# Performance work log

Measured on AMD Instinct MI355X. Metric: run time of the kernel, lower is better.

## Reference

```python
import jax, jax.numpy as jnp
import numpy as np

WS = 7          # window size (odd)
NUM_HEADS = 4


def _indices(H, W, ws):
    """Replicates get_attn_idx / get_bias_idx from the torch module (static numpy)."""
    H_, W_ = H - (ws - 1), W - (ws - 1)
    pad = ws // 2
    # unfold idx: flat key indices of each ws x ws window anchored at valid positions
    h_idx = np.tile(np.arange(W_), H_)
    w_idx = np.repeat(np.arange(H_), W_) * W
    k_idx = np.tile(np.arange(ws), ws) + np.repeat(np.arange(ws), ws) * W
    unfold = (h_idx + w_idx)[:, None] + k_idx            # [H_*W_, ws^2]
    # replication-pad the map of valid-window ids to size H x W
    amap = np.arange(H_ * W_).reshape(H_, W_)
    amap = np.pad(amap, pad, mode='edge').reshape(-1)    # [H*W]
    attn_idx = unfold[amap]                              # [H*W, ws^2]
    # relative-position bias indices
    nh = np.ones(ws, dtype=np.int64); nh[pad] = H - (ws - 1)
    nw = np.ones(ws, dtype=np.int64); nw[pad] = W - (ws - 1)
    ih = np.repeat(np.arange(ws), nh)                    # [H]
    iw = np.repeat(np.arange(ws), nw)                    # [W]
    idx_k = (np.arange(ws)[:, None] * (2 * ws - 1) + np.arange(ws)).reshape(-1)
    bias_hw = ih[:, None] * (2 * ws - 1) + iw            # [H, W]
    bias_idx = (bias_hw[..., None] + idx_k).reshape(-1, ws * ws)  # [H*W, ws^2]
    return jnp.asarray(attn_idx, jnp.int32), jnp.asarray(bias_idx, jnp.int32)


def setup_inputs() -> dict:
    key = jax.random.key(0)
    ks = jax.random.split(key, 6)
    B, C, H, W = 2, 64, 128, 128
    return {
        'x': jax.random.normal(ks[0], (B, C, H, W), jnp.float32),
        'qkv_w': jax.random.normal(ks[1], (3 * C, C), jnp.float32) * 0.05,
        'qkv_b': jax.random.normal(ks[2], (3 * C,), jnp.float32) * 0.05,
        'proj_w': jax.random.normal(ks[3], (C, C), jnp.float32) * 0.05,
        'proj_b': jax.random.normal(ks[4], (C,), jnp.float32) * 0.05,
        'relative_bias': jax.random.normal(ks[5], ((2 * WS - 1) ** 2, NUM_HEADS), jnp.float32) * 0.02,
    }


def reference(x, qkv_w, qkv_b, proj_w, proj_b, relative_bias):
    B, C, H, W = x.shape
    nH = NUM_HEADS
    hd = C // nH
    scale = hd ** -0.5
    attn_idx, bias_idx = _indices(H, W, WS)   # static int constants

    # 1x1 conv qkv
    qkv = jnp.einsum('bchw,oc->bohw', x, qkv_w) + qkv_b[None, :, None, None]
    qkv = qkv.reshape(B, 3, nH, hd, H * W)
    q = qkv[:, 0].transpose(0, 1, 3, 2) * scale          # [B,nH,HW,hd]
    k = qkv[:, 1].transpose(0, 1, 3, 2)
    v = qkv[:, 2].transpose(0, 1, 3, 2)

    kg = k[:, :, attn_idx]                               # [B,nH,HW,ws^2,hd]
    bias = relative_bias[bias_idx].transpose(2, 0, 1)    # [nH,HW,ws^2]
    attn = jnp.einsum('bhnd,bhnkd->bhnk', q, kg) + bias[None]
    attn = jax.nn.softmax(attn, axis=-1)

    out = jnp.einsum('bhnk,bhnkd->bhnd', attn, v[:, :, attn_idx])  # [B,nH,HW,hd]
    out = out.transpose(0, 1, 3, 2).reshape(B, C, H, W)

    out = jnp.einsum('bchw,oc->bohw', out, proj_w) + proj_b[None, :, None, None]
    return out
```

## Files before the change

kernel.cpp:

```cpp
#include <hip/hip_runtime.h>

#define HW 16384
#define NH 4
#define HD 16

__global__ __launch_bounds__(256) void qkv_kernel(
    const float* __restrict__ x, const float* __restrict__ w,
    const float* __restrict__ bias, float* __restrict__ qT,
    float* __restrict__ kT, float* __restrict__ vT)
{
  __shared__ float xs[64][72];
  int slice = blockIdx.x;
  int p0    = blockIdx.y * 64;
  int b     = blockIdx.z;
  int t     = threadIdx.x;

  {
    int c = t >> 2, f4 = t & 3;
    const float4* src = (const float4*)(x + (size_t)(b * 64 + c) * HW + p0);
    float4* dst = (float4*)(&xs[c][0]);
#pragma unroll
    for (int k2 = 0; k2 < 4; ++k2) dst[f4 * 4 + k2] = src[f4 * 4 + k2];
  }
  __syncthreads();

  int px = t & 63;
  int wv  = __builtin_amdgcn_readfirstlane(t >> 6);
  int o16 = slice * 4 + wv;
  int o0  = o16 * 16;
  int tsel = o16 >> 2;
  int h    = o16 & 3;

  float acc[16];
#pragma unroll
  for (int d = 0; d < 16; ++d) acc[d] = bias[o0 + d];

  for (int c4 = 0; c4 < 16; ++c4) {
    float a0 = xs[c4 * 4 + 0][px];
    float a1 = xs[c4 * 4 + 1][px];
    float a2 = xs[c4 * 4 + 2][px];
    float a3 = xs[c4 * 4 + 3][px];
#pragma unroll
    for (int d = 0; d < 16; ++d) {
      const float* wr = w + (o0 + d) * 64 + c4 * 4;
      acc[d] = fmaf(wr[0], a0, acc[d]);
      acc[d] = fmaf(wr[1], a1, acc[d]);
      acc[d] = fmaf(wr[2], a2, acc[d]);
      acc[d] = fmaf(wr[3], a3, acc[d]);
    }
  }
  if (tsel == 0) {
#pragma unroll
    for (int d = 0; d < 16; ++d) acc[d] *= 0.25f;
  }
  float* dst = (tsel == 0) ? qT : ((tsel == 1) ? kT : vT);
  float4* dp = (float4*)(dst + ((size_t)(b * NH + h) * HW + p0 + px) * HD);
  dp[0] = make_float4(acc[0], acc[1], acc[2], acc[3]);
  dp[1] = make_float4(acc[4], acc[5], acc[6], acc[7]);
  dp[2] = make_float4(acc[8], acc[9], acc[10], acc[11]);
  dp[3] = make_float4(acc[12], acc[13], acc[14], acc[15]);
}


__device__ __forceinline__ float4* swzp(float* buf, int px, int d4) {
  int off = (px << 6) ^ (((px & 7) ^ d4) << 4);
  return (float4*)((char*)buf + off);
}
__device__ __forceinline__ const float4* swzpc(const float* buf, int px, int d4) {
  int off = (px << 6) ^ (((px & 7) ^ d4) << 4);
  return (const float4*)((const char*)buf + off);
}

__global__ __launch_bounds__(256) void attn_kernel(
    const float* __restrict__ qT, const float* __restrict__ kT,
    const float* __restrict__ vT, const float* __restrict__ rb,
    float* __restrict__ attO)
{
  __shared__ float KV[484 * 16];
  __shared__ float rbl[169];

  int tile = blockIdx.x;
  int h    = blockIdx.y;
  int b    = blockIdx.z;
  int tx0  = (tile & 7) * 16;
  int ty0  = (tile >> 3) * 16;
  int oy   = ty0 - 3, ox = tx0 - 3;
  int t    = threadIdx.x;

  size_t base = (size_t)(b * NH + h) * HW;

  if (t < 169) rbl[t] = rb[t * NH + h];

  for (int idx = t; idx < 1936; idx += 256) {
    int pxi = idx >> 2, d4 = idx & 3;
    int r = pxi / 22, c = pxi % 22;
    int ra = oy + r; ra = ra < 0 ? 0 : (ra > 127 ? 127 : ra);
    int ca = ox + c; ca = ca < 0 ? 0 : (ca > 127 ? 127 : ca);
    size_t gp = (base + (size_t)ra * 128 + ca) * HD;
    *swzp(KV, pxi, d4) = ((const float4*)(kT + gp))[d4];
  }

  int lx = t & 15, ly = t >> 4;
  int y = ty0 + ly, xc = tx0 + lx;
  int sy = y - 3;  sy = sy < 0 ? 0 : (sy > 121 ? 121 : sy);
  int sx = xc - 3; sx = sx < 0 ? 0 : (sx > 121 ? 121 : sx);
  int li0 = sy - oy, lj0 = sx - ox;
  int ih = y - sy, iw = xc - sx;

  float qd[16];
  {
    const float4* qp = (const float4*)(qT + (base + (size_t)y * 128 + xc) * HD);
#pragma unroll
    for (int k = 0; k < 4; ++k) {
      float4 v = qp[k];
      qd[4 * k + 0] = v.x; qd[4 * k + 1] = v.y;
      qd[4 * k + 2] = v.z; qd[4 * k + 3] = v.w;
    }
  }

  __syncthreads();

  float lg[49];
#pragma unroll
  for (int i = 0; i < 7; ++i) {
#pragma unroll
    for (int j = 0; j < 7; ++j) {
      int px = (li0 + i) * 22 + (lj0 + j);
      float4 k0 = *swzpc(KV, px, 0);
      float4 k1 = *swzpc(KV, px, 1);
      float4 k2 = *swzpc(KV, px, 2);
      float4 k3 = *swzpc(KV, px, 3);
      float d;
      d = fmaf(qd[0], k0.x, rbl[(ih + i) * 13 + (iw + j)]);
      d = fmaf(qd[1], k0.y, d);  d = fmaf(qd[2], k0.z, d);
      d = fmaf(qd[3], k0.w, d);  d = fmaf(qd[4], k1.x, d);
      d = fmaf(qd[5], k1.y, d);  d = fmaf(qd[6], k1.z, d);
      d = fmaf(qd[7], k1.w, d);  d = fmaf(qd[8], k2.x, d);
      d = fmaf(qd[9], k2.y, d);  d = fmaf(qd[10], k2.z, d);
      d = fmaf(qd[11], k2.w, d); d = fmaf(qd[12], k3.x, d);
      d = fmaf(qd[13], k3.y, d); d = fmaf(qd[14], k3.z, d);
      d = fmaf(qd[15], k3.w, d);
      lg[i * 7 + j] = d;
    }
  }

  float mx = lg[0];
#pragma unroll
  for (int k = 1; k < 49; ++k) mx = fmaxf(mx, lg[k]);
  float s = 0.f;
#pragma unroll
  for (int k = 0; k < 49; ++k) { lg[k] = __expf(lg[k] - mx); s += lg[k]; }
  float inv = 1.f / s;

  __syncthreads();
  for (int idx = t; idx < 1936; idx += 256) {
    int pxi = idx >> 2, d4 = idx & 3;
    int r = pxi / 22, c = pxi % 22;
    int ra = oy + r; ra = ra < 0 ? 0 : (ra > 127 ? 127 : ra);
    int ca = ox + c; ca = ca < 0 ? 0 : (ca > 127 ? 127 : ca);
    size_t gp = (base + (size_t)ra * 128 + ca) * HD;
    *swzp(KV, pxi, d4) = ((const float4*)(vT + gp))[d4];
  }
  __syncthreads();

  float4 o0 = make_float4(0,0,0,0), o1 = o0, o2 = o0, o3 = o0;
#pragma unroll
  for (int i = 0; i < 7; ++i) {
#pragma unroll
    for (int j = 0; j < 7; ++j) {
      int px = (li0 + i) * 22 + (lj0 + j);
      float p = lg[i * 7 + j];
      float4 v0 = *swzpc(KV, px, 0);
      float4 v1 = *swzpc(KV, px, 1);
      float4 v2 = *swzpc(KV, px, 2);
      float4 v3 = *swzpc(KV, px, 3);
      o0.x = fmaf(p, v0.x, o0.x); o0.y = fmaf(p, v0.y, o0.y);
      o0.z = fmaf(p, v0.z, o0.z); o0.w = fmaf(p, v0.w, o0.w);
      o1.x = fmaf(p, v1.x, o1.x); o1.y = fmaf(p, v1.y, o1.y);
      o1.z = fmaf(p, v1.z, o1.z); o1.w = fmaf(p, v1.w, o1.w);
      o2.x = fmaf(p, v2.x, o2.x); o2.y = fmaf(p, v2.y, o2.y);
      o2.z = fmaf(p, v2.z, o2.z); o2.w = fmaf(p, v2.w, o2.w);
      o3.x = fmaf(p, v3.x, o3.x); o3.y = fmaf(p, v3.y, o3.y);
      o3.z = fmaf(p, v3.z, o3.z); o3.w = fmaf(p, v3.w, o3.w);
    }
  }

  size_t op = (size_t)y * 128 + xc;
  float* ob = attO + (size_t)b * 64 * HW + (size_t)h * 16 * HW + op;
  ob[0 * HW] = o0.x * inv;  ob[1 * HW] = o0.y * inv;
  ob[2 * HW] = o0.z * inv;  ob[3 * HW] = o0.w * inv;
  ob[4 * HW] = o1.x * inv;  ob[5 * HW] = o1.y * inv;
  ob[6 * HW] = o1.z * inv;  ob[7 * HW] = o1.w * inv;
  ob[8 * HW] = o2.x * inv;  ob[9 * HW] = o2.y * inv;
  ob[10 * HW] = o2.z * inv; ob[11 * HW] = o2.w * inv;
  ob[12 * HW] = o3.x * inv; ob[13 * HW] = o3.y * inv;
  ob[14 * HW] = o3.z * inv; ob[15 * HW] = o3.w * inv;
}

__global__ __launch_bounds__(256) void proj_kernel(
    const float* __restrict__ pw, const float* __restrict__ pb,
    float* __restrict__ out)
{
  __shared__ float as[64][72];
  int p0 = blockIdx.x * 64;
  int b  = blockIdx.y;
  int t  = threadIdx.x;

  {
    int c = t >> 2, f4 = t & 3;
    const float4* src = (const float4*)(out + (size_t)(b * 64 + c) * HW + p0);
    float4* dst = (float4*)(&as[c][0]);
#pragma unroll
    for (int k2 = 0; k2 < 4; ++k2) dst[f4 * 4 + k2] = src[f4 * 4 + k2];
  }
  __syncthreads();

  int px = t & 63;
  int og = __builtin_amdgcn_readfirstlane(t >> 6);
  float acc[16];
#pragma unroll
  for (int oo = 0; oo < 16; ++oo) acc[oo] = pb[og * 16 + oo];

  for (int c4 = 0; c4 < 16; ++c4) {
    float a0 = as[c4 * 4 + 0][px];
    float a1 = as[c4 * 4 + 1][px];
    float a2 = as[c4 * 4 + 2][px];
    float a3 = as[c4 * 4 + 3][px];
#pragma unroll
    for (int oo = 0; oo < 16; ++oo) {
      const float* wr = pw + (og * 16 + oo) * 64 + c4 * 4;
      acc[oo] = fmaf(wr[0], a0, acc[oo]);
      acc[oo] = fmaf(wr[1], a1, acc[oo]);
      acc[oo] = fmaf(wr[2], a2, acc[oo]);
      acc[oo] = fmaf(wr[3], a3, acc[oo]);
    }
  }
#pragma unroll
  for (int oo = 0; oo < 16; ++oo)
    out[((size_t)b * 64 + og * 16 + oo) * HW + p0 + px] = acc[oo];
}

extern "C" void kernel_launch(void* const* d_in, const int* in_sizes, int n_in,
                              void* d_out, int out_size, void* d_ws, size_t ws_size,
                              hipStream_t stream) {
  const float* x      = (const float*)d_in[0];
  const float* qkv_w  = (const float*)d_in[1];
  const float* qkv_b  = (const float*)d_in[2];
  const float* proj_w = (const float*)d_in[3];
  const float* proj_b = (const float*)d_in[4];
  const float* rb     = (const float*)d_in[5];
  float* out = (float*)d_out;

  const size_t TSZ = (size_t)2 * NH * HW * HD;
  float* qT = (float*)d_ws;
  float* kT = qT + TSZ;
  float* vT = kT + TSZ;

  qkv_kernel<<<dim3(3, 256, 2), 256, 0, stream>>>(x, qkv_w, qkv_b, qT, kT, vT);
  attn_kernel<<<dim3(64, NH, 2), 256, 0, stream>>>(qT, kT, vT, rb, out);
  proj_kernel<<<dim3(256, 2), 256, 0, stream>>>(proj_w, proj_b, out);
}
```

Baseline: 68.27 us.

## Use single-wave 8x8 attention tiles with padded LDS and no barriers

The attention kernel now runs one 64-thread wavefront per 8x8 pixel tile instead of 256 threads per 16x16 tile, launching four times as many blocks. Because each block is a single wave, all __syncthreads calls are dropped and the LDS halo is reloaded K then V without barriers. The XOR swizzle is replaced by a padded row stride of 20 floats. This cuts barrier stalls and raises scheduling flexibility, but the 14x14 halo per 64 pixels means proportionally more redundant global loads than the 22x22 halo per 256 pixels, and dropping the barriers assumes LDS accesses within one wavefront stay in program order.

```diff
diff --git a/kernel.cpp b/kernel.cpp
--- a/kernel.cpp
+++ b/kernel.cpp
@@ -61,46 +61,37 @@
   dp[3] = make_float4(acc[12], acc[13], acc[14], acc[15]);
 }
 
-
-__device__ __forceinline__ float4* swzp(float* buf, int px, int d4) {
-  int off = (px << 6) ^ (((px & 7) ^ d4) << 4);
-  return (float4*)((char*)buf + off);
-}
-__device__ __forceinline__ const float4* swzpc(const float* buf, int px, int d4) {
-  int off = (px << 6) ^ (((px & 7) ^ d4) << 4);
-  return (const float4*)((const char*)buf + off);
-}
-
-__global__ __launch_bounds__(256) void attn_kernel(
+#define PXS 20
+__global__ __launch_bounds__(64, 4) void attn_kernel(
     const float* __restrict__ qT, const float* __restrict__ kT,
     const float* __restrict__ vT, const float* __restrict__ rb,
     float* __restrict__ attO)
 {
-  __shared__ float KV[484 * 16];
+  __shared__ float KV[196 * PXS];
   __shared__ float rbl[169];
 
   int tile = blockIdx.x;
   int h    = blockIdx.y;
   int b    = blockIdx.z;
-  int tx0  = (tile & 7) * 16;
-  int ty0  = (tile >> 3) * 16;
+  int tx0  = (tile & 15) * 8;
+  int ty0  = (tile >> 4) * 8;
   int oy   = ty0 - 3, ox = tx0 - 3;
   int t    = threadIdx.x;
 
   size_t base = (size_t)(b * NH + h) * HW;
 
-  if (t < 169) rbl[t] = rb[t * NH + h];
-
-  for (int idx = t; idx < 1936; idx += 256) {
+  for (int i2 = t; i2 < 169; i2 += 64) rbl[i2] = rb[i2 * NH + h];
+
+  for (int idx = t; idx < 784; idx += 64) {
     int pxi = idx >> 2, d4 = idx & 3;
-    int r = pxi / 22, c = pxi % 22;
+    int r = pxi / 14, c = pxi % 14;
     int ra = oy + r; ra = ra < 0 ? 0 : (ra > 127 ? 127 : ra);
     int ca = ox + c; ca = ca < 0 ? 0 : (ca > 127 ? 127 : ca);
     size_t gp = (base + (size_t)ra * 128 + ca) * HD;
-    *swzp(KV, pxi, d4) = ((const float4*)(kT + gp))[d4];
-  }
-
-  int lx = t & 15, ly = t >> 4;
+    *(float4*)(&KV[pxi * PXS + d4 * 4]) = ((const float4*)(kT + gp))[d4];
+  }
+
+  int lx = t & 7, ly = t >> 3;
   int y = ty0 + ly, xc = tx0 + lx;
   int sy = y - 3;  sy = sy < 0 ? 0 : (sy > 121 ? 121 : sy);
   int sx = xc - 3; sx = sx < 0 ? 0 : (sx > 121 ? 121 : sx);
@@ -118,18 +109,17 @@
     }
   }
 
-  __syncthreads();
 
   float lg[49];
 #pragma unroll
   for (int i = 0; i < 7; ++i) {
 #pragma unroll
     for (int j = 0; j < 7; ++j) {
-      int px = (li0 + i) * 22 + (lj0 + j);
-      float4 k0 = *swzpc(KV, px, 0);
-      float4 k1 = *swzpc(KV, px, 1);
-      float4 k2 = *swzpc(KV, px, 2);
-      float4 k3 = *swzpc(KV, px, 3);
+      const float* kp = &KV[((li0 + i) * 14 + (lj0 + j)) * PXS];
+      float4 k0 = *(const float4*)(kp);
+      float4 k1 = *(const float4*)(kp + 4);
+      float4 k2 = *(const float4*)(kp + 8);
+      float4 k3 = *(const float4*)(kp + 12);
       float d;
       d = fmaf(qd[0], k0.x, rbl[(ih + i) * 13 + (iw + j)]);
       d = fmaf(qd[1], k0.y, d);  d = fmaf(qd[2], k0.z, d);
@@ -152,28 +142,26 @@
   for (int k = 0; k < 49; ++k) { lg[k] = __expf(lg[k] - mx); s += lg[k]; }
   float inv = 1.f / s;
 
-  __syncthreads();
-  for (int idx = t; idx < 1936; idx += 256) {
+  for (int idx = t; idx < 784; idx += 64) {
     int pxi = idx >> 2, d4 = idx & 3;
-    int r = pxi / 22, c = pxi % 22;
+    int r = pxi / 14, c = pxi % 14;
     int ra = oy + r; ra = ra < 0 ? 0 : (ra > 127 ? 127 : ra);
     int ca = ox + c; ca = ca < 0 ? 0 : (ca > 127 ? 127 : ca);
     size_t gp = (base + (size_t)ra * 128 + ca) * HD;
-    *swzp(KV, pxi, d4) = ((const float4*)(vT + gp))[d4];
-  }
-  __syncthreads();
+    *(float4*)(&KV[pxi * PXS + d4 * 4]) = ((const float4*)(vT + gp))[d4];
+  }
 
   float4 o0 = make_float4(0,0,0,0), o1 = o0, o2 = o0, o3 = o0;
 #pragma unroll
   for (int i = 0; i < 7; ++i) {
 #pragma unroll
     for (int j = 0; j < 7; ++j) {
-      int px = (li0 + i) * 22 + (lj0 + j);
+      const float* vp = &KV[((li0 + i) * 14 + (lj0 + j)) * PXS];
       float p = lg[i * 7 + j];
-      float4 v0 = *swzpc(KV, px, 0);
-      float4 v1 = *swzpc(KV, px, 1);
-      float4 v2 = *swzpc(KV, px, 2);
-      float4 v3 = *swzpc(KV, px, 3);
+      float4 v0 = *(const float4*)(vp);
+      float4 v1 = *(const float4*)(vp + 4);
+      float4 v2 = *(const float4*)(vp + 8);
+      float4 v3 = *(const float4*)(vp + 12);
       o0.x = fmaf(p, v0.x, o0.x); o0.y = fmaf(p, v0.y, o0.y);
       o0.z = fmaf(p, v0.z, o0.z); o0.w = fmaf(p, v0.w, o0.w);
       o1.x = fmaf(p, v1.x, o1.x); o1.y = fmaf(p, v1.y, o1.y);
@@ -185,8 +173,8 @@
     }
   }
 
-  size_t op = (size_t)y * 128 + xc;
-  float* ob = attO + (size_t)b * 64 * HW + (size_t)h * 16 * HW + op;
+  float* ob = attO + (size_t)b * 64 * HW + (size_t)h * 16 * HW
+            + (size_t)y * 128 + xc;
   ob[0 * HW] = o0.x * inv;  ob[1 * HW] = o0.y * inv;
   ob[2 * HW] = o0.z * inv;  ob[3 * HW] = o0.w * inv;
   ob[4 * HW] = o1.x * inv;  ob[5 * HW] = o1.y * inv;
@@ -257,6 +245,6 @@
   float* vT = kT + TSZ;
 
   qkv_kernel<<<dim3(3, 256, 2), 256, 0, stream>>>(x, qkv_w, qkv_b, qT, kT, vT);
-  attn_kernel<<<dim3(64, NH, 2), 256, 0, stream>>>(qT, kT, vT, rb, out);
+  attn_kernel<<<dim3(256, NH, 2), 64, 0, stream>>>(qT, kT, vT, rb, out);
   proj_kernel<<<dim3(256, 2), 256, 0, stream>>>(proj_w, proj_b, out);
 }
```

Measured after the change: 144.6 us. +111.8%, slower.
